# Optimization experiments

Hardware: AMD Instinct MI355X
Metric: run time of the kernel (lower is better)

The kernel has to match this reference:

```python
import jax, jax.numpy as jnp
import numpy as np

HW, WW, NH = 8, 8, 6  # window height/width, num heads


def _rel_pos_index(hw, ww):
    # Swin relative position index, computed statically with numpy
    coords = np.stack(np.meshgrid(np.arange(hw), np.arange(ww), indexing='ij'))  # [2,hw,ww]
    cf = coords.reshape(2, -1)
    rel = (cf[:, :, None] - cf[:, None, :]).transpose(1, 2, 0).astype(np.int64)  # [N,N,2]
    rel[:, :, 0] += hw - 1
    rel[:, :, 1] += ww - 1
    rel[:, :, 0] *= 2 * ww - 1
    return jnp.asarray(rel.sum(-1))  # [N,N]


def setup_inputs() -> dict:
    key = jax.random.key(0)
    ks = jax.random.split(key, 4)
    b, h, w, c = 8, 192, 192, 192
    return {
        'x': jax.random.normal(ks[0], (b, h * w, c), jnp.float32),
        'wqkv_w': jax.random.normal(ks[1], (c, 3 * c), jnp.float32) * 0.02,
        'wqkv_b': jnp.zeros((3 * c,), jnp.float32),
        'wp_w': jax.random.normal(ks[2], (c, c), jnp.float32) * 0.02,
        'wp_b': jnp.zeros((c,), jnp.float32),
        'bias_table': jax.random.normal(ks[3], ((2 * HW - 1) * (2 * WW - 1), NH), jnp.float32) * 0.02,
        'h': 192,
        'w': 192,
    }


def reference(x, wqkv_w, wqkv_b, wp_w, wp_b, bias_table, h, w):
    b, n, c = x.shape
    hd = c // NH
    pad_b = (HW - h % HW) % HW
    pad_r = (WW - w % WW) % WW
    H, W = h + pad_b, w + pad_r
    Hn, Wn = H // HW, W // WW
    N = HW * WW

    xi = x.reshape(b, h, w, c)
    xi = jnp.pad(xi, ((0, 0), (0, pad_b), (0, pad_r), (0, 0)))  # [b,H,W,c]

    qkv = xi @ wqkv_w + wqkv_b  # [b,H,W,3c]
    # partition into windows and split heads: -> [3, nW, NH, N, hd]
    qkv = qkv.reshape(b, Hn, HW, Wn, WW, 3, NH, hd)
    qkv = qkv.transpose(5, 0, 1, 3, 6, 2, 4, 7).reshape(3, b * Hn * Wn, NH, N, hd)
    q, k, v = qkv[0], qkv[1], qkv[2]

    idx = _rel_pos_index(HW, WW)  # [N,N]
    bias = bias_table[idx].transpose(2, 0, 1)  # [NH,N,N]

    scores = jnp.einsum('whqd,whkd->whqk', q, k) / np.sqrt(hd).astype(np.float32)
    scores = scores + bias[None]
    attn = jax.nn.softmax(scores, axis=-1)
    y = jnp.einsum('whqk,whkd->whqd', attn, v)  # [nW,NH,N,hd]

    # merge windows back to image: [b,H,W,c]
    y = y.reshape(b, Hn, Wn, NH, HW, WW, hd)
    y = y.transpose(0, 1, 4, 2, 5, 3, 6).reshape(b, H, W, c)
    out = y @ wp_w + wp_b
    out = out[:, :h, :w, :].reshape(b, h * w, c)
    return out
```

## Files before the change

### kernel.cpp

```cpp
#include <hip/hip_runtime.h>
#include <hip/hip_bf16.h>

typedef unsigned short u16;
typedef __attribute__((ext_vector_type(8))) short bf16x8;
typedef __attribute__((ext_vector_type(4))) float f32x4;
typedef __attribute__((ext_vector_type(2))) unsigned uint2v;

#define MFMA16(a, b, c) __builtin_amdgcn_mfma_f32_16x16x32_bf16(a, b, c, 0, 0, 0)

__device__ __forceinline__ u16 f2bf(float f) {
  union { float f; unsigned u; } v; v.f = f;
  unsigned r = v.u + 0x7fffu + ((v.u >> 16) & 1u);
  return (u16)(r >> 16);
}

__device__ __forceinline__ unsigned pkbf(float lo, float hi) {
  union { __hip_bfloat162 h; unsigned u; } v;
  v.h = __hip_bfloat162(__float2bfloat16(lo), __float2bfloat16(hi));
  return v.u;
}

__device__ __forceinline__ bf16x8 xform(f32x4 a0, f32x4 a1) {
  unsigned p0 = pkbf(a0[0], a0[1]), p1 = pkbf(a0[2], a0[3]);
  unsigned p2 = pkbf(a1[0], a1[1]), p3 = pkbf(a1[2], a1[3]);
  uint2v s02 = __builtin_amdgcn_permlane32_swap(p0, p2, false, false);
  uint2v w02 = __builtin_amdgcn_permlane16_swap(s02.x, s02.y, false, false);
  uint2v s13 = __builtin_amdgcn_permlane32_swap(p1, p3, false, false);
  uint2v w13 = __builtin_amdgcn_permlane16_swap(s13.x, s13.y, false, false);
  union { bf16x8 v; unsigned w[4]; } o;
  o.w[0] = w02.x; o.w[1] = w13.x; o.w[2] = w02.y; o.w[3] = w13.y;
  return o.v;
}

__device__ __forceinline__ float pmax16(float v) {
  union { float f; unsigned u; } a; a.f = v;
  uint2v r = __builtin_amdgcn_permlane16_swap(a.u, a.u, false, false);
  union { unsigned u; float f; } x, y; x.u = r.x; y.u = r.y;
  return fmaxf(x.f, y.f);
}
__device__ __forceinline__ float pmax32(float v) {
  union { float f; unsigned u; } a; a.f = v;
  uint2v r = __builtin_amdgcn_permlane32_swap(a.u, a.u, false, false);
  union { unsigned u; float f; } x, y; x.u = r.x; y.u = r.y;
  return fmaxf(x.f, y.f);
}
__device__ __forceinline__ float psum16(float v) {
  union { float f; unsigned u; } a; a.f = v;
  uint2v r = __builtin_amdgcn_permlane16_swap(a.u, a.u, false, false);
  union { unsigned u; float f; } x, y; x.u = r.x; y.u = r.y;
  return x.f + y.f;
}
__device__ __forceinline__ float psum32(float v) {
  union { float f; unsigned u; } a; a.f = v;
  uint2v r = __builtin_amdgcn_permlane32_swap(a.u, a.u, false, false);
  union { unsigned u; float f; } x, y; x.u = r.x; y.u = r.y;
  return x.f + y.f;
}

__global__ void pack_kernel(const float* __restrict__ wqkv_w,
                            const float* __restrict__ wp_w,
                            const float* __restrict__ bias_table,
                            u16* __restrict__ wpack, u16* __restrict__ wppack,
                            float* __restrict__ biasf) {
  int i = blockIdx.x * 256 + threadIdx.x;
  if (i < 110592) {
    int j = i & 7, l = (i >> 3) & 63;
    int rest = i >> 9;
    int ks = rest % 6, nt = rest / 6;
    int k = ks * 32 + (l >> 4) * 8 + j;
    int n = nt * 16 + (l & 15);
    wpack[i] = f2bf(wqkv_w[k * 576 + n]);
  } else if (i < 147456) {
    int i2 = i - 110592;
    int j = i2 & 7, l = (i2 >> 3) & 63;
    int rest = i2 >> 9;
    int ks = rest % 6, nt = rest / 6;
    int k = ks * 32 + (l >> 4) * 8 + j;
    int n = nt * 16 + (l & 15);
    wppack[i2] = f2bf(wp_w[k * 192 + n]);
  } else if (i < 172032) {
    int i2 = i - 147456;
    int r = i2 & 3, lane = (i2 >> 2) & 63, mt = (i2 >> 8) & 3, nt = (i2 >> 10) & 3, h = i2 >> 12;
    int q = nt * 16 + (lane & 15);
    int kk = mt * 16 + (lane >> 4) * 4 + r;
    int idx = ((q >> 3) - (kk >> 3) + 7) * 15 + ((q & 7) - (kk & 7) + 7);
    biasf[i2] = bias_table[idx * 6 + h];
  }
}

__global__ __launch_bounds__(128, 2) void attn6(
    const float* __restrict__ x, const u16* __restrict__ wpack,
    const float* __restrict__ wqkv_b, const float* __restrict__ biasf,
    u16* __restrict__ y) {
  __shared__ u16 xs[12288];
  const int lane = threadIdx.x & 63;
  const int wv = threadIdx.x >> 6;
  const int w = (blockIdx.x & 7) * 576 + (blockIdx.x >> 3);
  const int bb = w / 576, rem = w - bb * 576;
  const int wy = rem / 24, wx = rem - (rem / 24) * 24;
  const size_t xbase = (size_t)bb * 36864;
  const int g = lane >> 4, li = lane & 15;

  const int pix0 = (wy * 8 + (li >> 3)) * 192 + wx * 8 + (li & 7);
  const float* xr = x + (xbase + pix0) * 192 + g * 8;
  const u16* wbase = wpack + lane * 8;

  const float scale = 0.17677669529663687f;
  const f32x4 zero4 = {0.f, 0.f, 0.f, 0.f};

#pragma unroll
  for (int mi = 0; mi < 2; ++mi) {
    const int mt = wv * 2 + mi;
#pragma unroll
    for (int ks = 0; ks < 6; ++ks) {
      const float* p = xr + mt * 73728 + ks * 32;
      float4 f0 = *(const float4*)p;
      float4 f1 = *(const float4*)(p + 4);
      union { bf16x8 v; unsigned u[4]; } o;
      o.u[0] = pkbf(f0.x, f0.y); o.u[1] = pkbf(f0.z, f0.w);
      o.u[2] = pkbf(f1.x, f1.y); o.u[3] = pkbf(f1.z, f1.w);
      *(bf16x8*)(xs + ((mt * 6 + ks) * 64 + lane) * 8) = o.v;
    }
  }
  __syncthreads();

#pragma unroll 1
  for (int h = wv * 3; h < wv * 3 + 3; ++h) {
    f32x4 qt[2][4], kt[2][4], va[4][2];
#pragma unroll
    for (int i = 0; i < 2; ++i)
#pragma unroll
      for (int mt = 0; mt < 4; ++mt) { qt[i][mt] = zero4; kt[i][mt] = zero4; va[mt][i] = zero4; }
#pragma unroll
    for (int ks = 0; ks < 6; ++ks) {
      bf16x8 af[4];
#pragma unroll
      for (int mt = 0; mt < 4; ++mt)
        af[mt] = *(const bf16x8*)(xs + ((mt * 6 + ks) * 64 + lane) * 8);
#pragma unroll
      for (int i = 0; i < 2; ++i) {
        bf16x8 wq = *(const bf16x8*)(wbase + ((2 * h + i) * 6 + ks) * 512);
        bf16x8 wk = *(const bf16x8*)(wbase + ((12 + 2 * h + i) * 6 + ks) * 512);
        bf16x8 wvf = *(const bf16x8*)(wbase + ((24 + 2 * h + i) * 6 + ks) * 512);
#pragma unroll
        for (int mt = 0; mt < 4; ++mt) {
          qt[i][mt] = MFMA16(wq, af[mt], qt[i][mt]);
          kt[i][mt] = MFMA16(wk, af[mt], kt[i][mt]);
          va[mt][i] = MFMA16(af[mt], wvf, va[mt][i]);
        }
      }
    }

    f32x4 bq0 = *(const f32x4*)(wqkv_b + h * 32 + g * 4);
    f32x4 bq1 = *(const f32x4*)(wqkv_b + h * 32 + 16 + g * 4);
    f32x4 bk0 = *(const f32x4*)(wqkv_b + 192 + h * 32 + g * 4);
    f32x4 bk1 = *(const f32x4*)(wqkv_b + 192 + h * 32 + 16 + g * 4);
    bf16x8 qf[4], kf[4];
#pragma unroll
    for (int mt = 0; mt < 4; ++mt) {
      qf[mt] = xform((qt[0][mt] + bq0) * scale, (qt[1][mt] + bq1) * scale);
      kf[mt] = xform(kt[0][mt] + bk0, kt[1][mt] + bk1);
    }

    float bva0 = wqkv_b[384 + h * 32 + li], bva1 = wqkv_b[384 + h * 32 + 16 + li];
    bf16x8 vf[2][2];
#pragma unroll
    for (int i = 0; i < 2; ++i) {
      float bv = i ? bva1 : bva0;
#pragma unroll
      for (int ks2 = 0; ks2 < 2; ++ks2)
        vf[i][ks2] = xform(va[ks2 * 2][i] + bv, va[ks2 * 2 + 1][i] + bv);
    }

    const float* bfh = biasf + h * 4096 + lane * 4;
    f32x4 yt[2][4];
#pragma unroll
    for (int nt = 0; nt < 4; ++nt) { yt[0][nt] = zero4; yt[1][nt] = zero4; }
#pragma unroll
    for (int nt = 0; nt < 4; ++nt) {
      f32x4 em[4];
#pragma unroll
      for (int mt = 0; mt < 4; ++mt) {
        f32x4 stn = MFMA16(kf[mt], qf[nt], zero4);
        em[mt] = stn + *(const f32x4*)(bfh + (nt * 4 + mt) * 256);
      }
      float mx = -1e30f;
#pragma unroll
      for (int mt = 0; mt < 4; ++mt)
        mx = fmaxf(mx, fmaxf(fmaxf(em[mt][0], em[mt][1]), fmaxf(em[mt][2], em[mt][3])));
      mx = pmax16(mx);
      mx = pmax32(mx);
      float s = 0.f;
#pragma unroll
      for (int mt = 0; mt < 4; ++mt)
#pragma unroll
        for (int r = 0; r < 4; ++r) { em[mt][r] = __expf(em[mt][r] - mx); s += em[mt][r]; }
      s = psum16(s);
      s = psum32(s);
      float inv = 1.0f / s;
#pragma unroll
      for (int ks2 = 0; ks2 < 2; ++ks2) {
        bf16x8 pf = xform(em[ks2 * 2] * inv, em[ks2 * 2 + 1] * inv);
        yt[0][nt] = MFMA16(vf[0][ks2], pf, yt[0][nt]);
        yt[1][nt] = MFMA16(vf[1][ks2], pf, yt[1][nt]);
      }
    }

    u16* yp = y + (size_t)h * 9437184 + (xbase + pix0) * 32 + g * 8;
#pragma unroll
    for (int mt = 0; mt < 4; ++mt) {
      bf16x8 yfr = xform(yt[0][mt], yt[1][mt]);
      *(bf16x8*)(yp + mt * 12288) = yfr;
    }
  }
}

__global__ __launch_bounds__(256, 2) void proj_kernel(
    const u16* __restrict__ y, const u16* __restrict__ wppack,
    const float* __restrict__ wp_b, float* __restrict__ out) {
  const int tid = threadIdx.x;
  const int lane = tid & 63, wv = tid >> 6;
  const int g = lane >> 4, li = lane & 15;
  const size_t row0 = (size_t)blockIdx.x * 128 + wv * 32;
  const f32x4 zero4 = {0.f, 0.f, 0.f, 0.f};
  f32x4 acc[2][12];
#pragma unroll
  for (int mt = 0; mt < 2; ++mt)
#pragma unroll
    for (int nt = 0; nt < 12; ++nt) acc[mt][nt] = zero4;
#pragma unroll
  for (int ks = 0; ks < 6; ++ks) {
    bf16x8 af[2];
#pragma unroll
    for (int mt = 0; mt < 2; ++mt)
      af[mt] = *(const bf16x8*)(y + (size_t)ks * 9437184 + (row0 + mt * 16 + li) * 32 + g * 8);
#pragma unroll
    for (int nt = 0; nt < 12; ++nt) {
      bf16x8 bf = *(const bf16x8*)(wppack + (nt * 6 + ks) * 512 + lane * 8);
      acc[0][nt] = MFMA16(af[0], bf, acc[0][nt]);
      acc[1][nt] = MFMA16(af[1], bf, acc[1][nt]);
    }
  }
#pragma unroll
  for (int nt = 0; nt < 12; ++nt) {
    float bb = wp_b[nt * 16 + li];
#pragma unroll
    for (int mt = 0; mt < 2; ++mt)
#pragma unroll
      for (int r = 0; r < 4; ++r)
        out[(row0 + mt * 16 + g * 4 + r) * 192 + nt * 16 + li] = acc[mt][nt][r] + bb;
  }
}

extern "C" void kernel_launch(void* const* d_in, const int* in_sizes, int n_in,
                              void* d_out, int out_size, void* d_ws, size_t ws_size,
                              hipStream_t stream) {
  (void)in_sizes; (void)n_in; (void)out_size; (void)ws_size;
  const float* x          = (const float*)d_in[0];
  const float* wqkv_w     = (const float*)d_in[1];
  const float* wqkv_b     = (const float*)d_in[2];
  const float* wp_w       = (const float*)d_in[3];
  const float* wp_b       = (const float*)d_in[4];
  const float* bias_table = (const float*)d_in[5];
  float* out = (float*)d_out;
  char* ws = (char*)d_ws;
  u16* wpack   = (u16*)(ws);
  u16* wppack  = (u16*)(ws + 221184);
  float* biasf = (float*)(ws + 294912);
  u16* y       = (u16*)(ws + 393216);

  pack_kernel<<<672, 256, 0, stream>>>(wqkv_w, wp_w, bias_table, wpack, wppack, biasf);
  attn6<<<4608, 128, 0, stream>>>(x, wpack, wqkv_b, biasf, y);
  proj_kernel<<<2304, 256, 0, stream>>>(y, wppack, wp_b, out);
}
```

Measured before the change: 318.5 us.

## Split attention heads across blocks and fold bias into MFMA accumulator

The attention kernel now launches three blocks per window, each handling two heads (one per wave), instead of one block looping serially over three heads per wave. The block-to-window mapping keeps the three blocks for the same window on the same XCD, so repeated x reads are likely to hit L2. Bias is passed as the MFMA accumulator input rather than added afterwards, and each output tile is stored right after it is computed, which lowers register pressure. The cost is loading and converting the x window tile to bf16 three times instead of once.

```diff
diff --git a/kernel.cpp b/kernel.cpp
--- a/kernel.cpp
+++ b/kernel.cpp
@@ -95,7 +95,9 @@
   __shared__ u16 xs[12288];
   const int lane = threadIdx.x & 63;
   const int wv = threadIdx.x >> 6;
-  const int w = (blockIdx.x & 7) * 576 + (blockIdx.x >> 3);
+  const int fid = (blockIdx.x & 7) * 1728 + (blockIdx.x >> 3);
+  const int w = fid / 3, sub = fid - w * 3;
+  const int h = sub * 2 + wv;
   const int bb = w / 576, rem = w - bb * 576;
   const int wy = rem / 24, wx = rem - (rem / 24) * 24;
   const size_t xbase = (size_t)bb * 36864;
@@ -109,109 +111,97 @@
   const f32x4 zero4 = {0.f, 0.f, 0.f, 0.f};
 
 #pragma unroll
-  for (int mi = 0; mi < 2; ++mi) {
-    const int mt = wv * 2 + mi;
-#pragma unroll
-    for (int ks = 0; ks < 6; ++ks) {
-      const float* p = xr + mt * 73728 + ks * 32;
-      float4 f0 = *(const float4*)p;
-      float4 f1 = *(const float4*)(p + 4);
-      union { bf16x8 v; unsigned u[4]; } o;
-      o.u[0] = pkbf(f0.x, f0.y); o.u[1] = pkbf(f0.z, f0.w);
-      o.u[2] = pkbf(f1.x, f1.y); o.u[3] = pkbf(f1.z, f1.w);
-      *(bf16x8*)(xs + ((mt * 6 + ks) * 64 + lane) * 8) = o.v;
-    }
+  for (int ci = 0; ci < 12; ++ci) {
+    const int c = wv * 12 + ci, mt = c / 6, ks = c - (c / 6) * 6;
+    const float* p = xr + mt * 73728 + ks * 32;
+    float4 f0 = *(const float4*)p;
+    float4 f1 = *(const float4*)(p + 4);
+    union { bf16x8 v; unsigned u[4]; } o;
+    o.u[0] = pkbf(f0.x, f0.y); o.u[1] = pkbf(f0.z, f0.w);
+    o.u[2] = pkbf(f1.x, f1.y); o.u[3] = pkbf(f1.z, f1.w);
+    *(bf16x8*)(xs + ((mt * 6 + ks) * 64 + lane) * 8) = o.v;
   }
   __syncthreads();
 
-#pragma unroll 1
-  for (int h = wv * 3; h < wv * 3 + 3; ++h) {
-    f32x4 qt[2][4], kt[2][4], va[4][2];
-#pragma unroll
-    for (int i = 0; i < 2; ++i)
-#pragma unroll
-      for (int mt = 0; mt < 4; ++mt) { qt[i][mt] = zero4; kt[i][mt] = zero4; va[mt][i] = zero4; }
-#pragma unroll
-    for (int ks = 0; ks < 6; ++ks) {
-      bf16x8 af[4];
-#pragma unroll
-      for (int mt = 0; mt < 4; ++mt)
-        af[mt] = *(const bf16x8*)(xs + ((mt * 6 + ks) * 64 + lane) * 8);
-#pragma unroll
-      for (int i = 0; i < 2; ++i) {
-        bf16x8 wq = *(const bf16x8*)(wbase + ((2 * h + i) * 6 + ks) * 512);
-        bf16x8 wk = *(const bf16x8*)(wbase + ((12 + 2 * h + i) * 6 + ks) * 512);
-        bf16x8 wvf = *(const bf16x8*)(wbase + ((24 + 2 * h + i) * 6 + ks) * 512);
-#pragma unroll
-        for (int mt = 0; mt < 4; ++mt) {
-          qt[i][mt] = MFMA16(wq, af[mt], qt[i][mt]);
-          kt[i][mt] = MFMA16(wk, af[mt], kt[i][mt]);
-          va[mt][i] = MFMA16(af[mt], wvf, va[mt][i]);
-        }
+  f32x4 qt[2][4], kt[2][4], va[4][2];
+#pragma unroll
+  for (int i = 0; i < 2; ++i)
+#pragma unroll
+    for (int mt = 0; mt < 4; ++mt) { qt[i][mt] = zero4; kt[i][mt] = zero4; va[mt][i] = zero4; }
+#pragma unroll
+  for (int ks = 0; ks < 6; ++ks) {
+    bf16x8 af[4];
+#pragma unroll
+    for (int mt = 0; mt < 4; ++mt)
+      af[mt] = *(const bf16x8*)(xs + ((mt * 6 + ks) * 64 + lane) * 8);
+#pragma unroll
+    for (int i = 0; i < 2; ++i) {
+      bf16x8 wq = *(const bf16x8*)(wbase + ((2 * h + i) * 6 + ks) * 512);
+      bf16x8 wk = *(const bf16x8*)(wbase + ((12 + 2 * h + i) * 6 + ks) * 512);
+      bf16x8 wvf = *(const bf16x8*)(wbase + ((24 + 2 * h + i) * 6 + ks) * 512);
+#pragma unroll
+      for (int mt = 0; mt < 4; ++mt) {
+        qt[i][mt] = MFMA16(wq, af[mt], qt[i][mt]);
+        kt[i][mt] = MFMA16(wk, af[mt], kt[i][mt]);
+        va[mt][i] = MFMA16(af[mt], wvf, va[mt][i]);
       }
     }
-
-    f32x4 bq0 = *(const f32x4*)(wqkv_b + h * 32 + g * 4);
-    f32x4 bq1 = *(const f32x4*)(wqkv_b + h * 32 + 16 + g * 4);
-    f32x4 bk0 = *(const f32x4*)(wqkv_b + 192 + h * 32 + g * 4);
-    f32x4 bk1 = *(const f32x4*)(wqkv_b + 192 + h * 32 + 16 + g * 4);
-    bf16x8 qf[4], kf[4];
+  }
+
+  f32x4 bq0 = *(const f32x4*)(wqkv_b + h * 32 + g * 4);
+  f32x4 bq1 = *(const f32x4*)(wqkv_b + h * 32 + 16 + g * 4);
+  f32x4 bk0 = *(const f32x4*)(wqkv_b + 192 + h * 32 + g * 4);
+  f32x4 bk1 = *(const f32x4*)(wqkv_b + 192 + h * 32 + 16 + g * 4);
+  bf16x8 qf[4], kf[4];
+#pragma unroll
+  for (int mt = 0; mt < 4; ++mt) {
+    qf[mt] = xform((qt[0][mt] + bq0) * scale, (qt[1][mt] + bq1) * scale);
+    kf[mt] = xform(kt[0][mt] + bk0, kt[1][mt] + bk1);
+  }
+
+  float bva0 = wqkv_b[384 + h * 32 + li], bva1 = wqkv_b[384 + h * 32 + 16 + li];
+  bf16x8 vf[2][2];
+#pragma unroll
+  for (int i = 0; i < 2; ++i) {
+    float bv = i ? bva1 : bva0;
+#pragma unroll
+    for (int ks2 = 0; ks2 < 2; ++ks2)
+      vf[i][ks2] = xform(va[ks2 * 2][i] + bv, va[ks2 * 2 + 1][i] + bv);
+  }
+
+  const float* bfh = biasf + h * 4096 + lane * 4;
+  u16* yp = y + (size_t)h * 9437184 + (xbase + pix0) * 32 + g * 8;
+#pragma unroll
+  for (int nt = 0; nt < 4; ++nt) {
+    f32x4 em[4];
 #pragma unroll
     for (int mt = 0; mt < 4; ++mt) {
-      qf[mt] = xform((qt[0][mt] + bq0) * scale, (qt[1][mt] + bq1) * scale);
-      kf[mt] = xform(kt[0][mt] + bk0, kt[1][mt] + bk1);
-    }
-
-    float bva0 = wqkv_b[384 + h * 32 + li], bva1 = wqkv_b[384 + h * 32 + 16 + li];
-    bf16x8 vf[2][2];
-#pragma unroll
-    for (int i = 0; i < 2; ++i) {
-      float bv = i ? bva1 : bva0;
-#pragma unroll
-      for (int ks2 = 0; ks2 < 2; ++ks2)
-        vf[i][ks2] = xform(va[ks2 * 2][i] + bv, va[ks2 * 2 + 1][i] + bv);
-    }
-
-    const float* bfh = biasf + h * 4096 + lane * 4;
-    f32x4 yt[2][4];
-#pragma unroll
-    for (int nt = 0; nt < 4; ++nt) { yt[0][nt] = zero4; yt[1][nt] = zero4; }
-#pragma unroll
-    for (int nt = 0; nt < 4; ++nt) {
-      f32x4 em[4];
-#pragma unroll
-      for (int mt = 0; mt < 4; ++mt) {
-        f32x4 stn = MFMA16(kf[mt], qf[nt], zero4);
-        em[mt] = stn + *(const f32x4*)(bfh + (nt * 4 + mt) * 256);
-      }
-      float mx = -1e30f;
-#pragma unroll
-      for (int mt = 0; mt < 4; ++mt)
-        mx = fmaxf(mx, fmaxf(fmaxf(em[mt][0], em[mt][1]), fmaxf(em[mt][2], em[mt][3])));
-      mx = pmax16(mx);
-      mx = pmax32(mx);
-      float s = 0.f;
-#pragma unroll
-      for (int mt = 0; mt < 4; ++mt)
-#pragma unroll
-        for (int r = 0; r < 4; ++r) { em[mt][r] = __expf(em[mt][r] - mx); s += em[mt][r]; }
-      s = psum16(s);
-      s = psum32(s);
-      float inv = 1.0f / s;
-#pragma unroll
-      for (int ks2 = 0; ks2 < 2; ++ks2) {
-        bf16x8 pf = xform(em[ks2 * 2] * inv, em[ks2 * 2 + 1] * inv);
-        yt[0][nt] = MFMA16(vf[0][ks2], pf, yt[0][nt]);
-        yt[1][nt] = MFMA16(vf[1][ks2], pf, yt[1][nt]);
-      }
-    }
-
-    u16* yp = y + (size_t)h * 9437184 + (xbase + pix0) * 32 + g * 8;
-#pragma unroll
-    for (int mt = 0; mt < 4; ++mt) {
-      bf16x8 yfr = xform(yt[0][mt], yt[1][mt]);
-      *(bf16x8*)(yp + mt * 12288) = yfr;
-    }
+      f32x4 bias_c = *(const f32x4*)(bfh + (nt * 4 + mt) * 256);
+      em[mt] = MFMA16(kf[mt], qf[nt], bias_c);
+    }
+    float mx = -1e30f;
+#pragma unroll
+    for (int mt = 0; mt < 4; ++mt)
+      mx = fmaxf(mx, fmaxf(fmaxf(em[mt][0], em[mt][1]), fmaxf(em[mt][2], em[mt][3])));
+    mx = pmax16(mx);
+    mx = pmax32(mx);
+    float s = 0.f;
+#pragma unroll
+    for (int mt = 0; mt < 4; ++mt)
+#pragma unroll
+      for (int r = 0; r < 4; ++r) { em[mt][r] = __expf(em[mt][r] - mx); s += em[mt][r]; }
+    s = psum16(s);
+    s = psum32(s);
+    float inv = 1.0f / s;
+    f32x4 y0 = zero4, y1 = zero4;
+#pragma unroll
+    for (int ks2 = 0; ks2 < 2; ++ks2) {
+      bf16x8 pf = xform(em[ks2 * 2] * inv, em[ks2 * 2 + 1] * inv);
+      y0 = MFMA16(vf[0][ks2], pf, y0);
+      y1 = MFMA16(vf[1][ks2], pf, y1);
+    }
+    bf16x8 yfr = xform(y0, y1);
+    *(bf16x8*)(yp + nt * 12288) = yfr;
   }
 }
 
@@ -270,6 +260,6 @@
   u16* y       = (u16*)(ws + 393216);
 
   pack_kernel<<<672, 256, 0, stream>>>(wqkv_w, wp_w, bias_table, wpack, wppack, biasf);
-  attn6<<<4608, 128, 0, stream>>>(x, wpack, wqkv_b, biasf, y);
+  attn6<<<13824, 128, 0, stream>>>(x, wpack, wqkv_b, biasf, y);
   proj_kernel<<<2304, 256, 0, stream>>>(y, wppack, wp_b, out);
 }
```

Result: slower. 336.1 us (+5.5%).
